# Optimization experiments

Hardware: AMD Instinct MI355X
Metric: run time of the kernel (lower is better)

Reference implementation:

```python
import jax, jax.numpy as jnp
import numpy as np

B, N, T, E, H, R = 8, 64, 128, 128, 8, 4
DH = E // H


def setup_inputs() -> dict:
    key = jax.random.key(0)
    ks = jax.random.split(key, 14)
    s = 1.0 / np.sqrt(E)
    return {
        "node_memory": jax.random.normal(ks[0], (B, N, T, E), jnp.float32),
        "subgraph_memory": jax.random.normal(ks[1], (B, N, T, E, R - 1), jnp.float32),
        "Wq": jax.random.normal(ks[2], (E, E), jnp.float32) * s,
        "bq": jnp.zeros((E,), jnp.float32),
        "Wk": jax.random.normal(ks[3], (E, E), jnp.float32) * s,
        "bk": jnp.zeros((E,), jnp.float32),
        "Wv": jax.random.normal(ks[4], (E, E), jnp.float32) * s,
        "bv": jnp.zeros((E,), jnp.float32),
        "in_w": jax.random.normal(ks[5], (3 * E, E), jnp.float32) * s,
        "in_b": jnp.zeros((3 * E,), jnp.float32),
        "out_w": jax.random.normal(ks[6], (E, E), jnp.float32) * s,
        "out_b": jnp.zeros((E,), jnp.float32),
        "fc_w": jax.random.normal(ks[7], (E, R * E), jnp.float32) * (1.0 / np.sqrt(R * E)),
        "fc_b": jnp.zeros((E,), jnp.float32),
    }


def reference(node_memory, subgraph_memory, Wq, bq, Wk, bk, Wv, bv,
              in_w, in_b, out_w, out_b, fc_w, fc_b):
    # combined: [B,N,T,R,E] = concat(node[...,None,:], subgraph permuted)
    combined = jnp.concatenate(
        [node_memory[..., None, :], jnp.swapaxes(subgraph_memory, -1, -2)], axis=-2)
    # outer QKV projections
    Q = jnp.einsum("bntrf,ef->bntre", combined, Wq) + bq
    K = jnp.einsum("bntrf,ef->bntre", combined, Wk) + bk
    V = jnp.einsum("bntrf,ef->bntre", combined, Wv) + bv
    # nn.MultiheadAttention in-projection
    q = jnp.einsum("bntre,fe->bntrf", Q, in_w[:E]) + in_b[:E]
    k = jnp.einsum("bntre,fe->bntrf", K, in_w[E:2 * E]) + in_b[E:2 * E]
    v = jnp.einsum("bntre,fe->bntrf", V, in_w[2 * E:]) + in_b[2 * E:]
    # split heads: [B,N,T,R,H,DH]
    q = q.reshape(B, N, T, R, H, DH) * (1.0 / np.sqrt(DH))
    k = k.reshape(B, N, T, R, H, DH)
    v = v.reshape(B, N, T, R, H, DH)
    scores = jnp.einsum("bntrhd,bntshd->bnthrs", q, k)  # [B,N,T,H,R,R]
    attn = jax.nn.softmax(scores, axis=-1)
    o = jnp.einsum("bnthrs,bntshd->bntrhd", attn, v).reshape(B, N, T, R, E)
    o = jnp.einsum("bntre,fe->bntrf", o, out_w) + out_b
    # concat the R representations and fuse
    o = o.reshape(B, N, T, R * E)
    return jnp.einsum("bntc,ec->bnte", o, fc_w) + fc_b
```

## Files before the change

kernel.cpp:

```cpp
#include <hip/hip_runtime.h>
#include <hip/hip_bf16.h>

constexpr int cE  = 128;
constexpr int cR  = 4;
constexpr int cNT = 65536;

typedef short s8v  __attribute__((ext_vector_type(8)));
typedef unsigned short u8v __attribute__((ext_vector_type(8)));
typedef float f4v  __attribute__((ext_vector_type(4)));

static __device__ __forceinline__ unsigned short f2bf(float x) {
    union { float f; unsigned int u; } v; v.f = x;
    unsigned int r = v.u + 0x7fffu + ((v.u >> 16) & 1u);
    return (unsigned short)(r >> 16);
}
static __device__ __forceinline__ float bf2f(unsigned short u) {
    union { unsigned int u; float f; } v; v.u = ((unsigned int)u) << 16;
    return v.f;
}

__global__ __launch_bounds__(256) void k_prep(
    const float* __restrict__ Wq, const float* __restrict__ Wk, const float* __restrict__ Wv,
    const float* __restrict__ in_w, const float* __restrict__ out_w, const float* __restrict__ fc_w,
    const float* __restrict__ bq, const float* __restrict__ bk, const float* __restrict__ bv,
    const float* __restrict__ in_b, const float* __restrict__ out_b, const float* __restrict__ fc_b,
    unsigned short* __restrict__ wqkv, unsigned short* __restrict__ meff,
    float* __restrict__ bqkv, float* __restrict__ beff)
{
    int bid = blockIdx.x;
    if (bid < 448) {
        int idx = bid * 256 + threadIdx.x;
        if (idx < 3 * cE * cE) {
            int w   = idx >> 14;
            int rem = idx & (cE * cE - 1);
            int f = rem >> 7, g = rem & 127;
            const float* Wsel = (w == 0) ? Wq : ((w == 1) ? Wk : Wv);
            const float* iw = in_w + (size_t)(w * cE + f) * cE;
            float s = 0.f;
            #pragma unroll 4
            for (int e = 0; e < cE; ++e) s += iw[e] * Wsel[e * cE + g];
            if (w == 0) s *= 0.25f;
            wqkv[idx] = f2bf(s);
        } else {
            int i2 = idx - 3 * cE * cE;
            int e1 = i2 >> 9;
            int c  = i2 & 511;
            const float* fw = fc_w + (size_t)e1 * 512 + (c >> 7) * cE;
            int ee = c & 127;
            float s = 0.f;
            #pragma unroll 4
            for (int f = 0; f < cE; ++f) s += fw[f] * out_w[f * cE + ee];
            meff[(size_t)e1 * 512 + c] = f2bf(s);
        }
    } else {
        int idx = (bid - 448) * 256 + threadIdx.x;
        if (idx < 384) {
            int w = idx >> 7, f = idx & 127;
            const float* bsel = (w == 0) ? bq : ((w == 1) ? bk : bv);
            const float* iw = in_w + (size_t)(w * cE + f) * cE;
            float s = 0.f;
            for (int e = 0; e < cE; ++e) s += iw[e] * bsel[e];
            s += in_b[w * cE + f];
            if (w == 0) s *= 0.25f;
            bqkv[idx] = s;
        } else {
            int f = idx - 384;
            float s = 0.f;
            for (int c = 0; c < 512; ++c) s += fc_w[(size_t)f * 512 + c] * out_b[c & 127];
            beff[f] = s + fc_b[f];
        }
    }
}

#define TOKB   32
#define TOKC   8
#define PITCH  136
#define OPITCH 520

__global__ __launch_bounds__(256) void k_main(
    const float* __restrict__ node, const float* __restrict__ sub,
    const unsigned short* __restrict__ wqkv,
    const unsigned short* __restrict__ meff,
    const float* __restrict__ bqkv,
    const float* __restrict__ beff,
    float* __restrict__ out)
{
    __shared__ unsigned short uAO[32 * PITCH];
    __shared__ unsigned short sQKV[3][cR * TOKC][PITCH];
    __shared__ float sBias[3 * cE];

    const int tid  = threadIdx.x;
    const int lane = tid & 63;
    const int wv   = tid >> 6;
    const int l15  = lane & 15;
    const int lq   = lane >> 4;
    const int ct0  = wv * 2;

    for (int i = tid; i < 3 * cE; i += 256) sBias[i] = bqkv[i];

    const int tokBlock = blockIdx.x * TOKB;

    for (int chunk = 0; chunk < TOKB / TOKC; ++chunk) {
        const int tokBase = tokBlock + chunk * TOKC;
        __syncthreads();

        {
            int tok = tid >> 5;
            int e4  = (tid & 31) * 4;
            float4 v = *(const float4*)(node + (size_t)(tokBase + tok) * cE + e4);
            ushort4 w4;
            w4.x = f2bf(v.x); w4.y = f2bf(v.y); w4.z = f2bf(v.z); w4.w = f2bf(v.w);
            *(ushort4*)&uAO[(tok * cR) * PITCH + e4] = w4;
        }
        #pragma unroll
        for (int it = 0; it < 3; ++it) {
            int i4  = tid + it * 256;
            int tok = i4 / 96;
            int p0  = (i4 - tok * 96) * 4;
            float4 v = *(const float4*)(sub + (size_t)(tokBase + tok) * 384 + p0);
            float vv[4] = {v.x, v.y, v.z, v.w};
            #pragma unroll
            for (int c = 0; c < 4; ++c) {
                int p = p0 + c;
                int e = p / 3, j = p - e * 3;
                uAO[(tok * cR + 1 + j) * PITCH + e] = f2bf(vv[c]);
            }
        }
        __syncthreads();

        for (int w = 0; w < 3; ++w) {
            const unsigned short* wbase = wqkv + (size_t)w * cE * cE;
            f4v acc[2][2];
            #pragma unroll
            for (int a = 0; a < 2; ++a)
                #pragma unroll
                for (int b = 0; b < 2; ++b) acc[a][b] = (f4v){0.f, 0.f, 0.f, 0.f};
            #pragma unroll
            for (int kc = 0; kc < 4; ++kc) {
                int koff = kc * 32 + lq * 8;
                s8v a0 = *(const s8v*)&uAO[(0 * 16 + l15) * PITCH + koff];
                s8v a1 = *(const s8v*)&uAO[(1 * 16 + l15) * PITCH + koff];
                #pragma unroll
                for (int c = 0; c < 2; ++c) {
                    int f = (ct0 + c) * 16 + l15;
                    s8v b = *(const s8v*)(wbase + (size_t)f * cE + koff);
                    acc[0][c] = __builtin_amdgcn_mfma_f32_16x16x32_bf16(a0, b, acc[0][c], 0, 0, 0);
                    acc[1][c] = __builtin_amdgcn_mfma_f32_16x16x32_bf16(a1, b, acc[1][c], 0, 0, 0);
                }
            }
            #pragma unroll
            for (int rt = 0; rt < 2; ++rt)
                #pragma unroll
                for (int c = 0; c < 2; ++c) {
                    int f = (ct0 + c) * 16 + l15;
                    float bias = sBias[w * cE + f];
                    #pragma unroll
                    for (int i = 0; i < 4; ++i) {
                        int row = rt * 16 + lq * 4 + i;
                        sQKV[w][row][f] = f2bf(acc[rt][c][i] + bias);
                    }
                }
        }
        __syncthreads();

        {
            int tok = tid >> 5;
            int h   = (tid >> 2) & 7;
            int r   = tid & 3;
            const unsigned short* qp = &sQKV[0][tok * cR + r][h * 16];
            u8v q0 = *(const u8v*)qp, q1 = *(const u8v*)(qp + 8);
            float q[16];
            #pragma unroll
            for (int d = 0; d < 8; ++d) { q[d] = bf2f(q0[d]); q[8 + d] = bf2f(q1[d]); }
            float sc[4];
            #pragma unroll
            for (int s = 0; s < 4; ++s) {
                const unsigned short* kp = &sQKV[1][tok * cR + s][h * 16];
                u8v k0 = *(const u8v*)kp, k1 = *(const u8v*)(kp + 8);
                float t = 0.f;
                #pragma unroll
                for (int d = 0; d < 8; ++d) t += q[d] * bf2f(k0[d]) + q[8 + d] * bf2f(k1[d]);
                sc[s] = t;
            }
            float m = fmaxf(fmaxf(sc[0], sc[1]), fmaxf(sc[2], sc[3]));
            float p[4], l = 0.f;
            #pragma unroll
            for (int s = 0; s < 4; ++s) { p[s] = __expf(sc[s] - m); l += p[s]; }
            float inv = 1.f / l;
            float o[16];
            #pragma unroll
            for (int d = 0; d < 16; ++d) o[d] = 0.f;
            #pragma unroll
            for (int s = 0; s < 4; ++s) {
                float w = p[s] * inv;
                const unsigned short* vp = &sQKV[2][tok * cR + s][h * 16];
                u8v v0 = *(const u8v*)vp, v1 = *(const u8v*)(vp + 8);
                #pragma unroll
                for (int d = 0; d < 8; ++d) { o[d] += w * bf2f(v0[d]); o[8 + d] += w * bf2f(v1[d]); }
            }
            unsigned int pk[8];
            #pragma unroll
            for (int d2 = 0; d2 < 8; ++d2)
                pk[d2] = (unsigned int)f2bf(o[2 * d2]) | ((unsigned int)f2bf(o[2 * d2 + 1]) << 16);
            uint4* op = (uint4*)&uAO[tok * OPITCH + r * cE + h * 16];
            op[0] = make_uint4(pk[0], pk[1], pk[2], pk[3]);
            op[1] = make_uint4(pk[4], pk[5], pk[6], pk[7]);
        }
        __syncthreads();

        {
            f4v acc[2];
            acc[0] = (f4v){0.f, 0.f, 0.f, 0.f};
            acc[1] = (f4v){0.f, 0.f, 0.f, 0.f};
            int arow = l15 & 7;
            #pragma unroll 4
            for (int kc = 0; kc < 16; ++kc) {
                int koff = kc * 32 + lq * 8;
                s8v a = *(const s8v*)&uAO[arow * OPITCH + koff];
                #pragma unroll
                for (int c = 0; c < 2; ++c) {
                    int e1 = (ct0 + c) * 16 + l15;
                    s8v b = *(const s8v*)(meff + (size_t)e1 * 512 + koff);
                    acc[c] = __builtin_amdgcn_mfma_f32_16x16x32_bf16(a, b, acc[c], 0, 0, 0);
                }
            }
            if (lq < 2) {
                #pragma unroll
                for (int c = 0; c < 2; ++c) {
                    int e1 = (ct0 + c) * 16 + l15;
                    float bb = beff[e1];
                    #pragma unroll
                    for (int i = 0; i < 4; ++i) {
                        int tok = lq * 4 + i;
                        out[(size_t)(tokBase + tok) * cE + e1] = acc[c][i] + bb;
                    }
                }
            }
        }
    }
}

extern "C" void kernel_launch(void* const* d_in, const int* in_sizes, int n_in,
                              void* d_out, int out_size, void* d_ws, size_t ws_size,
                              hipStream_t stream) {
    const float* node  = (const float*)d_in[0];
    const float* sub   = (const float*)d_in[1];
    const float* Wq    = (const float*)d_in[2];
    const float* bq    = (const float*)d_in[3];
    const float* Wk    = (const float*)d_in[4];
    const float* bk    = (const float*)d_in[5];
    const float* Wv    = (const float*)d_in[6];
    const float* bv    = (const float*)d_in[7];
    const float* in_w  = (const float*)d_in[8];
    const float* in_b  = (const float*)d_in[9];
    const float* out_w = (const float*)d_in[10];
    const float* out_b = (const float*)d_in[11];
    const float* fc_w  = (const float*)d_in[12];
    const float* fc_b  = (const float*)d_in[13];

    unsigned short* ws_wqkv = (unsigned short*)d_ws;
    unsigned short* ws_meff = ws_wqkv + 3 * cE * cE;
    float* ws_bqkv = (float*)((char*)d_ws + (size_t)(3 * cE * cE + cE * cR * cE) * 2);
    float* ws_beff = ws_bqkv + 3 * cE;

    k_prep<<<dim3(450), dim3(256), 0, stream>>>(Wq, Wk, Wv, in_w, out_w, fc_w,
                                                bq, bk, bv, in_b, out_b, fc_b,
                                                ws_wqkv, ws_meff, ws_bqkv, ws_beff);
    k_main<<<dim3(cNT / TOKB), dim3(256), 0, stream>>>(node, sub, ws_wqkv, ws_meff,
                                                       ws_bqkv, ws_beff, (float*)d_out);
}
```

Baseline: 346.1 us.

## Split prep dot products across lanes, vectorize subgraph load and MFMA epilogue stores

The weight-folding prep kernel now splits each 128-long dot product across four lanes and reduces with shuffles, launching four times more blocks for more parallelism. The subgraph-memory transpose load reads three float4s per thread and writes packed ushort4 rows instead of scattered scalar LDS stores. The MFMA operands are swapped so each lane holds four consecutive output columns, which lets the QKV epilogue write ushort4 to LDS and the final output write float4 to global memory instead of strided scalars. Correctness depends on the swapped operand layout matching the transposed indexing.

```diff
diff --git a/kernel.cpp b/kernel.cpp
--- a/kernel.cpp
+++ b/kernel.cpp
@@ -28,32 +28,49 @@
     float* __restrict__ bqkv, float* __restrict__ beff)
 {
     int bid = blockIdx.x;
-    if (bid < 448) {
-        int idx = bid * 256 + threadIdx.x;
-        if (idx < 3 * cE * cE) {
-            int w   = idx >> 14;
-            int rem = idx & (cE * cE - 1);
+    if (bid < 1792) {
+        int gt = bid * 256 + (int)threadIdx.x;
+        int o  = gt >> 2;
+        int p  = gt & 3;
+        float s;
+        if (o < 3 * cE * cE) {
+            int w   = o >> 14;
+            int rem = o & (cE * cE - 1);
             int f = rem >> 7, g = rem & 127;
             const float* Wsel = (w == 0) ? Wq : ((w == 1) ? Wk : Wv);
-            const float* iw = in_w + (size_t)(w * cE + f) * cE;
-            float s = 0.f;
-            #pragma unroll 4
-            for (int e = 0; e < cE; ++e) s += iw[e] * Wsel[e * cE + g];
+            const float* iw = in_w + (size_t)(w * cE + f) * cE + p * 32;
+            const float* wp = Wsel + (size_t)(p * 32) * cE + g;
+            float s0 = 0.f, s1 = 0.f;
+            #pragma unroll
+            for (int e = 0; e < 32; e += 2) {
+                s0 += iw[e]     * wp[(size_t)e * cE];
+                s1 += iw[e + 1] * wp[(size_t)(e + 1) * cE];
+            }
+            s = s0 + s1;
+            s += __shfl_xor(s, 1);
+            s += __shfl_xor(s, 2);
             if (w == 0) s *= 0.25f;
-            wqkv[idx] = f2bf(s);
+            if (p == 0) wqkv[o] = f2bf(s);
         } else {
-            int i2 = idx - 3 * cE * cE;
+            int i2 = o - 3 * cE * cE;
             int e1 = i2 >> 9;
             int c  = i2 & 511;
-            const float* fw = fc_w + (size_t)e1 * 512 + (c >> 7) * cE;
+            const float* fw = fc_w + (size_t)e1 * 512 + (c >> 7) * cE + p * 32;
             int ee = c & 127;
-            float s = 0.f;
-            #pragma unroll 4
-            for (int f = 0; f < cE; ++f) s += fw[f] * out_w[f * cE + ee];
-            meff[(size_t)e1 * 512 + c] = f2bf(s);
+            const float* ow = out_w + (size_t)(p * 32) * cE + ee;
+            float s0 = 0.f, s1 = 0.f;
+            #pragma unroll
+            for (int ff = 0; ff < 32; ff += 2) {
+                s0 += fw[ff]     * ow[(size_t)ff * cE];
+                s1 += fw[ff + 1] * ow[(size_t)(ff + 1) * cE];
+            }
+            s = s0 + s1;
+            s += __shfl_xor(s, 1);
+            s += __shfl_xor(s, 2);
+            if (p == 0) meff[i2] = f2bf(s);
         }
     } else {
-        int idx = (bid - 448) * 256 + threadIdx.x;
+        int idx = (bid - 1792) * 256 + (int)threadIdx.x;
         if (idx < 384) {
             int w = idx >> 7, f = idx & 127;
             const float* bsel = (w == 0) ? bq : ((w == 1) ? bk : bv);
@@ -108,23 +125,23 @@
             int tok = tid >> 5;
             int e4  = (tid & 31) * 4;
             float4 v = *(const float4*)(node + (size_t)(tokBase + tok) * cE + e4);
-            ushort4 w4;
-            w4.x = f2bf(v.x); w4.y = f2bf(v.y); w4.z = f2bf(v.z); w4.w = f2bf(v.w);
-            *(ushort4*)&uAO[(tok * cR) * PITCH + e4] = w4;
-        }
-        #pragma unroll
-        for (int it = 0; it < 3; ++it) {
-            int i4  = tid + it * 256;
-            int tok = i4 / 96;
-            int p0  = (i4 - tok * 96) * 4;
-            float4 v = *(const float4*)(sub + (size_t)(tokBase + tok) * 384 + p0);
-            float vv[4] = {v.x, v.y, v.z, v.w};
-            #pragma unroll
-            for (int c = 0; c < 4; ++c) {
-                int p = p0 + c;
-                int e = p / 3, j = p - e * 3;
-                uAO[(tok * cR + 1 + j) * PITCH + e] = f2bf(vv[c]);
-            }
+            *(ushort4*)&uAO[(tok * cR) * PITCH + e4] =
+                make_ushort4(f2bf(v.x), f2bf(v.y), f2bf(v.z), f2bf(v.w));
+        }
+        {
+            int tok = tid >> 5;
+            int eg  = tid & 31;
+            const float* sp = sub + (size_t)(tokBase + tok) * 384 + eg * 12;
+            float4 f0 = *(const float4*)(sp + 0);
+            float4 f1 = *(const float4*)(sp + 4);
+            float4 f2 = *(const float4*)(sp + 8);
+            int e0 = eg * 4;
+            *(ushort4*)&uAO[(tok * cR + 1) * PITCH + e0] =
+                make_ushort4(f2bf(f0.x), f2bf(f0.w), f2bf(f1.z), f2bf(f2.y));
+            *(ushort4*)&uAO[(tok * cR + 2) * PITCH + e0] =
+                make_ushort4(f2bf(f0.y), f2bf(f1.x), f2bf(f1.w), f2bf(f2.z));
+            *(ushort4*)&uAO[(tok * cR + 3) * PITCH + e0] =
+                make_ushort4(f2bf(f0.z), f2bf(f1.y), f2bf(f2.x), f2bf(f2.w));
         }
         __syncthreads();
 
@@ -144,21 +161,21 @@
                 for (int c = 0; c < 2; ++c) {
                     int f = (ct0 + c) * 16 + l15;
                     s8v b = *(const s8v*)(wbase + (size_t)f * cE + koff);
-                    acc[0][c] = __builtin_amdgcn_mfma_f32_16x16x32_bf16(a0, b, acc[0][c], 0, 0, 0);
-                    acc[1][c] = __builtin_amdgcn_mfma_f32_16x16x32_bf16(a1, b, acc[1][c], 0, 0, 0);
+                    acc[0][c] = __builtin_amdgcn_mfma_f32_16x16x32_bf16(b, a0, acc[0][c], 0, 0, 0);
+                    acc[1][c] = __builtin_amdgcn_mfma_f32_16x16x32_bf16(b, a1, acc[1][c], 0, 0, 0);
                 }
             }
             #pragma unroll
             for (int rt = 0; rt < 2; ++rt)
                 #pragma unroll
                 for (int c = 0; c < 2; ++c) {
-                    int f = (ct0 + c) * 16 + l15;
-                    float bias = sBias[w * cE + f];
-                    #pragma unroll
-                    for (int i = 0; i < 4; ++i) {
-                        int row = rt * 16 + lq * 4 + i;
-                        sQKV[w][row][f] = f2bf(acc[rt][c][i] + bias);
-                    }
+                    int col = (ct0 + c) * 16 + lq * 4;
+                    float4 b4 = *(const float4*)&sBias[w * cE + col];
+                    *(ushort4*)&sQKV[w][rt * 16 + l15][col] =
+                        make_ushort4(f2bf(acc[rt][c][0] + b4.x),
+                                     f2bf(acc[rt][c][1] + b4.y),
+                                     f2bf(acc[rt][c][2] + b4.z),
+                                     f2bf(acc[rt][c][3] + b4.w));
                 }
         }
         __syncthreads();
@@ -221,19 +238,18 @@
                 for (int c = 0; c < 2; ++c) {
                     int e1 = (ct0 + c) * 16 + l15;
                     s8v b = *(const s8v*)(meff + (size_t)e1 * 512 + koff);
-                    acc[c] = __builtin_amdgcn_mfma_f32_16x16x32_bf16(a, b, acc[c], 0, 0, 0);
-                }
-            }
-            if (lq < 2) {
-                #pragma unroll
-                for (int c = 0; c < 2; ++c) {
-                    int e1 = (ct0 + c) * 16 + l15;
-                    float bb = beff[e1];
-                    #pragma unroll
-                    for (int i = 0; i < 4; ++i) {
-                        int tok = lq * 4 + i;
-                        out[(size_t)(tokBase + tok) * cE + e1] = acc[c][i] + bb;
-                    }
+                    acc[c] = __builtin_amdgcn_mfma_f32_16x16x32_bf16(b, a, acc[c], 0, 0, 0);
+                }
+            }
+            if (l15 < 8) {
+                size_t tokOff = (size_t)(tokBase + l15) * cE;
+                #pragma unroll
+                for (int c = 0; c < 2; ++c) {
+                    int col = (ct0 + c) * 16 + lq * 4;
+                    float4 b4 = *(const float4*)&beff[col];
+                    *(float4*)&out[tokOff + col] =
+                        make_float4(acc[c][0] + b4.x, acc[c][1] + b4.y,
+                                    acc[c][2] + b4.z, acc[c][3] + b4.w);
                 }
             }
         }
@@ -263,9 +279,9 @@
     float* ws_bqkv = (float*)((char*)d_ws + (size_t)(3 * cE * cE + cE * cR * cE) * 2);
     float* ws_beff = ws_bqkv + 3 * cE;
 
-    k_prep<<<dim3(450), dim3(256), 0, stream>>>(Wq, Wk, Wv, in_w, out_w, fc_w,
-                                                bq, bk, bv, in_b, out_b, fc_b,
-                                                ws_wqkv, ws_meff, ws_bqkv, ws_beff);
+    k_prep<<<dim3(1794), dim3(256), 0, stream>>>(Wq, Wk, Wv, in_w, out_w, fc_w,
+                                                 bq, bk, bv, in_b, out_b, fc_b,
+                                                 ws_wqkv, ws_meff, ws_bqkv, ws_beff);
     k_main<<<dim3(cNT / TOKB), dim3(256), 0, stream>>>(node, sub, ws_wqkv, ws_meff,
                                                        ws_bqkv, ws_beff, (float*)d_out);
 }
```

New measurement: 347.8 us. About the same (+0.5%).
